# Kernel optimization log

Measured on AMD Instinct MI355X. Metric: run time of the kernel, lower is better.

Reference implementation:

```python
import jax, jax.numpy as jnp
import numpy as np

B, LP, LC = 1, 640, 128
NODE, HID, PAIR = 128, 32, 128
EPS = 1e-5

def _unif(key, shape, fan_in):
    s = 1.0 / np.sqrt(fan_in)
    return jax.random.uniform(key, shape, jnp.float32, -s, s)

def setup_inputs() -> dict:
    key = jax.random.key(0)
    ks = jax.random.split(key, 8)
    return {
        "p_embed": jax.random.normal(ks[0], (B, LP, NODE), jnp.float32),
        "c_embed": jax.random.normal(ks[1], (B, LC, NODE), jnp.float32),
        "p_mask": jnp.ones((B, LP), dtype=bool),
        "c_mask": jnp.ones((B, LC), dtype=bool),
        "ln_p_w": jnp.ones((NODE,), jnp.float32),
        "ln_p_b": jnp.zeros((NODE,), jnp.float32),
        "ln_c_w": jnp.ones((NODE,), jnp.float32),
        "ln_c_b": jnp.zeros((NODE,), jnp.float32),
        "W_p": _unif(ks[2], (HID, NODE), NODE),
        "b_p": _unif(ks[3], (HID,), NODE),
        "W_c": _unif(ks[4], (HID, NODE), NODE),
        "b_c": _unif(ks[5], (HID,), NODE),
        "W_out": _unif(ks[6], (PAIR, HID * HID), HID * HID),
        "b_out": _unif(ks[7], (PAIR,), HID * HID),
    }

def _layernorm(x, w, b):
    m = jnp.mean(x, axis=-1, keepdims=True)
    v = jnp.mean(jnp.square(x - m), axis=-1, keepdims=True)
    return (x - m) * jax.lax.rsqrt(v + EPS) * w + b

def reference(p_embed, c_embed, p_mask, c_mask,
              ln_p_w, ln_p_b, ln_c_w, ln_c_b,
              W_p, b_p, W_c, b_c, W_out, b_out):
    # inter_mask[b,i,j] = p_mask[b,i] & c_mask[b,j]
    inter_mask = p_mask[..., :, None] & c_mask[..., None, :]
    p = _layernorm(p_embed, ln_p_w, ln_p_b)
    c = _layernorm(c_embed, ln_c_w, ln_c_b)
    p = p @ W_p.T + b_p  # [B, LP, HID]
    c = c @ W_c.T + b_c  # [B, LC, HID]
    # torch: einsum('...bc,...de->...bdce') -> flatten(-2) -> Linear(HID^2, PAIR)
    # flat index = c*HID + e, so W_out[k, c*HID+e] == W3[k, c, e].
    # Fold linear_out into the outer product: out[b,i,j,k] = sum_{c,e} p[b,i,c] q[b,j,e] W3[k,c,e]
    W3 = W_out.reshape(PAIR, HID, HID)
    out = jnp.einsum('bic,kce->bike', p, W3)          # [B, LP, PAIR, HID]
    out = jnp.einsum('bike,bje->bijk', out, c)        # [B, LP, LC, PAIR]
    out = (out + b_out) * inter_mask[..., None].astype(out.dtype)
    return out, inter_mask
```

## Files before the change

kernel.cpp:

```cpp
#include <hip/hip_runtime.h>
#include <hip/hip_bf16.h>

#define LP   640
#define LC   128
#define NODE 128
#define HID  32
#define PAIR 128
#define EPS  1e-5f

typedef __bf16 bf16_t;
typedef __attribute__((ext_vector_type(8))) __bf16 bf16x8;
typedef __attribute__((ext_vector_type(4))) float f32x4;

__global__ __launch_bounds__(128) void k1_rows(
    const float* __restrict__ p_embed, const float* __restrict__ c_embed,
    const int* __restrict__ p_mask, const int* __restrict__ c_mask,
    const float* __restrict__ ln_p_w, const float* __restrict__ ln_p_b,
    const float* __restrict__ ln_c_w, const float* __restrict__ ln_c_b,
    const float* __restrict__ W_p, const float* __restrict__ b_p,
    const float* __restrict__ W_c, const float* __restrict__ b_c,
    bf16_t* __restrict__ p_out, bf16_t* __restrict__ c_out,
    float* __restrict__ mask_out)
{
    const int blk = blockIdx.x;
    const int t = threadIdx.x;

    if (blk >= LP + LC) {
        int base = (blk - (LP + LC)) * 256;
        #pragma unroll
        for (int u = 0; u < 2; ++u) {
            int idx = base + u * 128 + t;
            int i = idx >> 7, j = idx & 127;
            mask_out[idx] = (p_mask[i] != 0 && c_mask[j] != 0) ? 1.0f : 0.0f;
        }
        return;
    }

    const float* x; const float* lw; const float* lb;
    const float* W; const float* bb; bf16_t* yo;
    if (blk < LP) {
        x = p_embed + blk * NODE; lw = ln_p_w; lb = ln_p_b;
        W = W_p; bb = b_p; yo = p_out + blk * HID;
    } else {
        int row = blk - LP;
        x = c_embed + row * NODE; lw = ln_c_w; lb = ln_c_b;
        W = W_c; bb = b_c; yo = c_out + row * HID;
    }

    __shared__ __align__(16) float sx[NODE];
    __shared__ __align__(16) float red[NODE];

    float v = x[t];
    red[t] = v;
    __syncthreads();
    #pragma unroll
    for (int s = 64; s > 0; s >>= 1) {
        if (t < s) red[t] += red[t + s];
        __syncthreads();
    }
    float mean = red[0] * (1.0f / NODE);
    float d = v - mean;
    __syncthreads();
    red[t] = d * d;
    __syncthreads();
    #pragma unroll
    for (int s = 64; s > 0; s >>= 1) {
        if (t < s) red[t] += red[t + s];
        __syncthreads();
    }
    float var = red[0] * (1.0f / NODE);
    float xn = d * rsqrtf(var + EPS) * lw[t] + lb[t];
    __syncthreads();
    sx[t] = xn;
    __syncthreads();

    int h = t & 31, seg = t >> 5;
    const f32x4* wv = (const f32x4*)(W + h * NODE + seg * 32);
    const f32x4* xv = (const f32x4*)(sx + seg * 32);
    float acc = 0.f;
    #pragma unroll
    for (int z = 0; z < 8; ++z) {
        f32x4 a = wv[z], b = xv[z];
        acc += a[0]*b[0] + a[1]*b[1] + a[2]*b[2] + a[3]*b[3];
    }
    red[t] = acc;
    __syncthreads();
    if (t < 32) {
        float y = red[t] + red[t + 32] + red[t + 64] + red[t + 96] + bb[t];
        yo[t] = (bf16_t)y;
    }
}

__global__ __launch_bounds__(64) void k2_s(
    const bf16_t* __restrict__ c_b, const float* __restrict__ W_out,
    bf16_t* __restrict__ S2)
{
    const int k = blockIdx.x;
    const int lane = threadIdx.x;
    const int q = lane >> 4, l16 = lane & 15;
    const float* Wrow = W_out + k * (HID * HID);

    f32x4 zacc = {0.f, 0.f, 0.f, 0.f};

    bf16x8 bfrag[2];
    #pragma unroll
    for (int nt = 0; nt < 2; ++nt) {
        int c = nt * 16 + l16;
        const float* wp = Wrow + c * 32 + q * 8;
        f32x4 w0 = *(const f32x4*)(wp);
        f32x4 w1 = *(const f32x4*)(wp + 4);
        bf16x8 bf;
        #pragma unroll
        for (int z = 0; z < 4; ++z) { bf[z] = (bf16_t)w0[z]; bf[z + 4] = (bf16_t)w1[z]; }
        bfrag[nt] = bf;
    }

    #pragma unroll
    for (int mt = 0; mt < 8; ++mt) {
        bf16x8 afrag = *(const bf16x8*)(c_b + (mt * 16 + l16) * 32 + q * 8);
        f32x4 acc0 = __builtin_amdgcn_mfma_f32_16x16x32_bf16(afrag, bfrag[0], zacc, 0, 0, 0);
        f32x4 acc1 = __builtin_amdgcn_mfma_f32_16x16x32_bf16(afrag, bfrag[1], zacc, 0, 0, 0);
        #pragma unroll
        for (int r = 0; r < 4; ++r) {
            int jrow = mt * 16 + q * 4 + r;
            S2[(jrow * 128 + k) * 32 + l16]      = (bf16_t)acc0[r];
            S2[(jrow * 128 + k) * 32 + 16 + l16] = (bf16_t)acc1[r];
        }
    }
}

__global__ __launch_bounds__(256) void k3_main(
    const bf16_t* __restrict__ p_b, const bf16_t* __restrict__ S2,
    const float* __restrict__ b_out,
    const int* __restrict__ p_mask, const int* __restrict__ c_mask,
    float* __restrict__ out)
{
    const int blk = blockIdx.x;
    const int bn = blk & 255;
    const int bi = blk >> 8;
    const int wave = threadIdx.x >> 6;
    const int lane = threadIdx.x & 63;
    const int q = lane >> 4, l16 = lane & 15;
    const int i0 = bi * 64 + wave * 16;
    const int n0 = bn * 64;

    f32x4 zacc = {0.f, 0.f, 0.f, 0.f};

    bf16x8 afrag = *(const bf16x8*)(p_b + (i0 + l16) * 32 + q * 8);

    f32x4 acc[4];
    #pragma unroll
    for (int t = 0; t < 4; ++t) {
        bf16x8 bfrag = *(const bf16x8*)(S2 + (n0 + t * 16 + l16) * 32 + q * 8);
        acc[t] = __builtin_amdgcn_mfma_f32_16x16x32_bf16(afrag, bfrag, zacc, 0, 0, 0);
    }

    const int j = n0 >> 7;
    const float cm = (c_mask[j] != 0) ? 1.f : 0.f;
    float pm[4];
    #pragma unroll
    for (int r = 0; r < 4; ++r)
        pm[r] = ((p_mask[i0 + q * 4 + r] != 0) ? 1.f : 0.f) * cm;

    #pragma unroll
    for (int t = 0; t < 4; ++t) {
        int n = n0 + t * 16 + l16;
        float bo = b_out[n & 127];
        #pragma unroll
        for (int r = 0; r < 4; ++r) {
            int i = i0 + q * 4 + r;
            out[i * (LC * PAIR) + n] = (acc[t][r] + bo) * pm[r];
        }
    }
}

extern "C" void kernel_launch(void* const* d_in, const int* in_sizes, int n_in,
                              void* d_out, int out_size, void* d_ws, size_t ws_size,
                              hipStream_t stream) {
    const float* p_embed = (const float*)d_in[0];
    const float* c_embed = (const float*)d_in[1];
    const int* p_mask = (const int*)d_in[2];
    const int* c_mask = (const int*)d_in[3];
    const float* ln_p_w = (const float*)d_in[4];
    const float* ln_p_b = (const float*)d_in[5];
    const float* ln_c_w = (const float*)d_in[6];
    const float* ln_c_b = (const float*)d_in[7];
    const float* W_p   = (const float*)d_in[8];
    const float* b_p   = (const float*)d_in[9];
    const float* W_c   = (const float*)d_in[10];
    const float* b_c   = (const float*)d_in[11];
    const float* W_out = (const float*)d_in[12];
    const float* b_out = (const float*)d_in[13];

    bf16_t* p_b = (bf16_t*)d_ws;
    bf16_t* c_b = (bf16_t*)((char*)d_ws + 40960);
    bf16_t* S2  = (bf16_t*)((char*)d_ws + 49152);

    float* out = (float*)d_out;
    float* mask_out = out + (size_t)LP * LC * PAIR;

    k1_rows<<<LP + LC + 320, 128, 0, stream>>>(
        p_embed, c_embed, p_mask, c_mask,
        ln_p_w, ln_p_b, ln_c_w, ln_c_b,
        W_p, b_p, W_c, b_c, p_b, c_b, mask_out);

    k2_s<<<PAIR, 64, 0, stream>>>(c_b, W_out, S2);

    k3_main<<<2560, 256, 0, stream>>>(p_b, S2, b_out, p_mask, c_mask, out);
}
```

Measured before the change: 104.6 us.

## Use wave-per-row layernorm, split k2 across more blocks, widen k3 tiles

k1 now processes four rows per block, one wave each, and replaces the shared-memory tree reductions with wave shuffles computing sum and sum-of-squares in one pass. The mask writes are vectorised to float4. k2 is split four ways per output channel to raise parallelism, and k3 handles a full 128-column j-slice per block with bias values hoisted. Together these cut synchronisation and launch overhead across three kernels. The single-pass variance is slightly less numerically robust.

```diff
diff --git a/kernel.cpp b/kernel.cpp
--- a/kernel.cpp
+++ b/kernel.cpp
@@ -12,7 +12,7 @@
 typedef __attribute__((ext_vector_type(8))) __bf16 bf16x8;
 typedef __attribute__((ext_vector_type(4))) float f32x4;
 
-__global__ __launch_bounds__(128) void k1_rows(
+__global__ __launch_bounds__(256) void k1_rows(
     const float* __restrict__ p_embed, const float* __restrict__ c_embed,
     const int* __restrict__ p_mask, const int* __restrict__ c_mask,
     const float* __restrict__ ln_p_w, const float* __restrict__ ln_p_b,
@@ -25,77 +25,70 @@
     const int blk = blockIdx.x;
     const int t = threadIdx.x;
 
-    if (blk >= LP + LC) {
-        int base = (blk - (LP + LC)) * 256;
-        #pragma unroll
-        for (int u = 0; u < 2; ++u) {
-            int idx = base + u * 128 + t;
-            int i = idx >> 7, j = idx & 127;
-            mask_out[idx] = (p_mask[i] != 0 && c_mask[j] != 0) ? 1.0f : 0.0f;
-        }
+    if (blk >= 192) {
+        int idx = (blk - 192) * 1024 + t * 4;
+        int i = idx >> 7, j = idx & 127;
+        float pm = (p_mask[i] != 0) ? 1.0f : 0.0f;
+        f32x4 m;
+        m[0] = pm * ((c_mask[j + 0] != 0) ? 1.0f : 0.0f);
+        m[1] = pm * ((c_mask[j + 1] != 0) ? 1.0f : 0.0f);
+        m[2] = pm * ((c_mask[j + 2] != 0) ? 1.0f : 0.0f);
+        m[3] = pm * ((c_mask[j + 3] != 0) ? 1.0f : 0.0f);
+        *(f32x4*)(mask_out + idx) = m;
         return;
     }
+
+    const int wave = t >> 6;
+    const int lane = t & 63;
+    const int row = blk * 4 + wave;
 
     const float* x; const float* lw; const float* lb;
     const float* W; const float* bb; bf16_t* yo;
-    if (blk < LP) {
-        x = p_embed + blk * NODE; lw = ln_p_w; lb = ln_p_b;
-        W = W_p; bb = b_p; yo = p_out + blk * HID;
+    if (row < LP) {
+        x = p_embed + row * NODE; lw = ln_p_w; lb = ln_p_b;
+        W = W_p; bb = b_p; yo = p_out + row * HID;
     } else {
-        int row = blk - LP;
-        x = c_embed + row * NODE; lw = ln_c_w; lb = ln_c_b;
-        W = W_c; bb = b_c; yo = c_out + row * HID;
-    }
-
-    __shared__ __align__(16) float sx[NODE];
-    __shared__ __align__(16) float red[NODE];
-
-    float v = x[t];
-    red[t] = v;
+        int r = row - LP;
+        x = c_embed + r * NODE; lw = ln_c_w; lb = ln_c_b;
+        W = W_c; bb = b_c; yo = c_out + r * HID;
+    }
+
+    __shared__ __align__(16) float sx[4][NODE];
+
+    float v0 = x[lane], v1 = x[lane + 64];
+    float s  = v0 + v1;
+    float ss = v0 * v0 + v1 * v1;
+    #pragma unroll
+    for (int off = 32; off > 0; off >>= 1) {
+        s  += __shfl_xor(s, off);
+        ss += __shfl_xor(ss, off);
+    }
+    float mean = s * (1.0f / NODE);
+    float var  = ss * (1.0f / NODE) - mean * mean;
+    float rs   = rsqrtf(var + EPS);
+    sx[wave][lane]      = (v0 - mean) * rs * lw[lane]      + lb[lane];
+    sx[wave][lane + 64] = (v1 - mean) * rs * lw[lane + 64] + lb[lane + 64];
     __syncthreads();
-    #pragma unroll
-    for (int s = 64; s > 0; s >>= 1) {
-        if (t < s) red[t] += red[t + s];
-        __syncthreads();
-    }
-    float mean = red[0] * (1.0f / NODE);
-    float d = v - mean;
-    __syncthreads();
-    red[t] = d * d;
-    __syncthreads();
-    #pragma unroll
-    for (int s = 64; s > 0; s >>= 1) {
-        if (t < s) red[t] += red[t + s];
-        __syncthreads();
-    }
-    float var = red[0] * (1.0f / NODE);
-    float xn = d * rsqrtf(var + EPS) * lw[t] + lb[t];
-    __syncthreads();
-    sx[t] = xn;
-    __syncthreads();
-
-    int h = t & 31, seg = t >> 5;
-    const f32x4* wv = (const f32x4*)(W + h * NODE + seg * 32);
-    const f32x4* xv = (const f32x4*)(sx + seg * 32);
+
+    const int h = lane & 31, half = lane >> 5;
+    const f32x4* wv = (const f32x4*)(W + h * NODE + half * 64);
+    const f32x4* xv = (const f32x4*)(&sx[wave][half * 64]);
     float acc = 0.f;
     #pragma unroll
-    for (int z = 0; z < 8; ++z) {
+    for (int z = 0; z < 16; ++z) {
         f32x4 a = wv[z], b = xv[z];
         acc += a[0]*b[0] + a[1]*b[1] + a[2]*b[2] + a[3]*b[3];
     }
-    red[t] = acc;
-    __syncthreads();
-    if (t < 32) {
-        float y = red[t] + red[t + 32] + red[t + 64] + red[t + 96] + bb[t];
-        yo[t] = (bf16_t)y;
-    }
+    acc += __shfl_xor(acc, 32);
+    if (lane < 32) yo[h] = (bf16_t)(acc + bb[h]);
 }
 
 __global__ __launch_bounds__(64) void k2_s(
     const bf16_t* __restrict__ c_b, const float* __restrict__ W_out,
     bf16_t* __restrict__ S2)
 {
-    const int k = blockIdx.x;
+    const int k = blockIdx.x >> 2;
+    const int mtbase = (blockIdx.x & 3) * 2;
     const int lane = threadIdx.x;
     const int q = lane >> 4, l16 = lane & 15;
     const float* Wrow = W_out + k * (HID * HID);
@@ -116,7 +109,8 @@
     }
 
     #pragma unroll
-    for (int mt = 0; mt < 8; ++mt) {
+    for (int mi = 0; mi < 2; ++mi) {
+        int mt = mtbase + mi;
         bf16x8 afrag = *(const bf16x8*)(c_b + (mt * 16 + l16) * 32 + q * 8);
         f32x4 acc0 = __builtin_amdgcn_mfma_f32_16x16x32_bf16(afrag, bfrag[0], zacc, 0, 0, 0);
         f32x4 acc1 = __builtin_amdgcn_mfma_f32_16x16x32_bf16(afrag, bfrag[1], zacc, 0, 0, 0);
@@ -136,40 +130,43 @@
     float* __restrict__ out)
 {
     const int blk = blockIdx.x;
-    const int bn = blk & 255;
-    const int bi = blk >> 8;
+    const int bn = blk & 127;
+    const int bi = blk >> 7;
     const int wave = threadIdx.x >> 6;
     const int lane = threadIdx.x & 63;
     const int q = lane >> 4, l16 = lane & 15;
     const int i0 = bi * 64 + wave * 16;
-    const int n0 = bn * 64;
+    const int n0 = bn * 128;
 
     f32x4 zacc = {0.f, 0.f, 0.f, 0.f};
 
     bf16x8 afrag = *(const bf16x8*)(p_b + (i0 + l16) * 32 + q * 8);
 
-    f32x4 acc[4];
-    #pragma unroll
-    for (int t = 0; t < 4; ++t) {
+    f32x4 acc[8];
+    #pragma unroll
+    for (int t = 0; t < 8; ++t) {
         bf16x8 bfrag = *(const bf16x8*)(S2 + (n0 + t * 16 + l16) * 32 + q * 8);
         acc[t] = __builtin_amdgcn_mfma_f32_16x16x32_bf16(afrag, bfrag, zacc, 0, 0, 0);
     }
 
-    const int j = n0 >> 7;
+    const int j = bn;
     const float cm = (c_mask[j] != 0) ? 1.f : 0.f;
     float pm[4];
     #pragma unroll
     for (int r = 0; r < 4; ++r)
         pm[r] = ((p_mask[i0 + q * 4 + r] != 0) ? 1.f : 0.f) * cm;
 
-    #pragma unroll
-    for (int t = 0; t < 4; ++t) {
+    float bo[8];
+    #pragma unroll
+    for (int t = 0; t < 8; ++t) bo[t] = b_out[t * 16 + l16];
+
+    #pragma unroll
+    for (int t = 0; t < 8; ++t) {
         int n = n0 + t * 16 + l16;
-        float bo = b_out[n & 127];
         #pragma unroll
         for (int r = 0; r < 4; ++r) {
             int i = i0 + q * 4 + r;
-            out[i * (LC * PAIR) + n] = (acc[t][r] + bo) * pm[r];
+            out[(size_t)i * (LC * PAIR) + n] = (acc[t][r] + bo[t]) * pm[r];
         }
     }
 }
@@ -199,12 +196,12 @@
     float* out = (float*)d_out;
     float* mask_out = out + (size_t)LP * LC * PAIR;
 
-    k1_rows<<<LP + LC + 320, 128, 0, stream>>>(
+    k1_rows<<<272, 256, 0, stream>>>(
         p_embed, c_embed, p_mask, c_mask,
         ln_p_w, ln_p_b, ln_c_w, ln_c_b,
         W_p, b_p, W_c, b_c, p_b, c_b, mask_out);
 
-    k2_s<<<PAIR, 64, 0, stream>>>(c_b, W_out, S2);
-
-    k3_main<<<2560, 256, 0, stream>>>(p_b, S2, b_out, p_mask, c_mask, out);
-}
+    k2_s<<<512, 64, 0, stream>>>(c_b, W_out, S2);
+
+    k3_main<<<1280, 256, 0, stream>>>(p_b, S2, b_out, p_mask, c_mask, out);
+}
```

New measurement: 103.8 us. No clear change (-0.8%).
